# Performance work log

Measured on AMD Instinct MI355X. Metric: run time of the kernel, lower is better.

Reference implementation:

```python
import jax, jax.numpy as jnp
import numpy as np

B, T, F, H = 1024, 512, 64, 128


def setup_inputs() -> dict:
    key = jax.random.key(0)
    ks = jax.random.split(key, 9)
    s_ih = 1.0 / np.sqrt(H)
    inp = {
        "x": jax.random.normal(ks[0], (B, T, F), dtype=jnp.float32),
        # PyTorch GRU packed weights: [3H, F] and [3H, H], gate order (r, z, n)
        "W_ih": jax.random.uniform(ks[1], (3 * H, F), minval=-s_ih, maxval=s_ih, dtype=jnp.float32),
        "W_hh": jax.random.uniform(ks[2], (3 * H, H), minval=-s_ih, maxval=s_ih, dtype=jnp.float32),
        "b_ih": jax.random.uniform(ks[3], (3 * H,), minval=-s_ih, maxval=s_ih, dtype=jnp.float32),
        "b_hh": jax.random.uniform(ks[4], (3 * H,), minval=-s_ih, maxval=s_ih, dtype=jnp.float32),
        "W1": jax.random.uniform(ks[5], (32, H), minval=-1 / np.sqrt(H), maxval=1 / np.sqrt(H), dtype=jnp.float32),
        "b1": jax.random.uniform(ks[6], (32,), minval=-1 / np.sqrt(H), maxval=1 / np.sqrt(H), dtype=jnp.float32),
        "W2": jax.random.uniform(ks[7], (1, 32), minval=-1 / np.sqrt(32), maxval=1 / np.sqrt(32), dtype=jnp.float32),
        "b2": jax.random.uniform(ks[8], (1,), minval=-1 / np.sqrt(32), maxval=1 / np.sqrt(32), dtype=jnp.float32),
    }
    return inp


def _gru_last_hidden(x, W_ih, W_hh, b_ih, b_hh):
    # Precompute input-side gate pre-activations for all timesteps: [B, T, 3H]
    xg = jnp.einsum("btf,gf->btg", x, W_ih) + b_ih
    h0 = jnp.zeros((x.shape[0], W_hh.shape[1]), dtype=x.dtype)

    def step(h, xg_t):
        hg = h @ W_hh.T + b_hh  # [B, 3H]
        xr, xz, xn = jnp.split(xg_t, 3, axis=-1)
        hr, hz, hn = jnp.split(hg, 3, axis=-1)
        r = jax.nn.sigmoid(xr + hr)
        z = jax.nn.sigmoid(xz + hz)
        n = jnp.tanh(xn + r * hn)
        h_new = (1.0 - z) * n + z * h
        return h_new, None

    hT, _ = jax.lax.scan(step, h0, jnp.swapaxes(xg, 0, 1))  # scan over T
    return hT  # [B, H]


def reference(x, W_ih, W_hh, b_ih, b_hh, W1, b1, W2, b2):
    hT = _gru_last_hidden(x, W_ih, W_hh, b_ih, b_hh)
    hidden = jax.nn.relu(hT @ W1.T + b1)  # [B, 32]; dropout is identity at inference
    out = hidden @ W2.T + b2  # [B, 1]
    return out.squeeze(-1)  # [B]
```

## Files before the change

### kernel.cpp

```cpp
#include <hip/hip_runtime.h>
#include <math.h>


#define Bsz  1024
#define Tlen 512
#define Fdim 64
#define Hdim 128
#define Gdim 384
#define NB   8
#define NTHR 512
#define NBLK (Bsz / NB)

typedef __attribute__((ext_vector_type(8))) _Float16 f16x8;
typedef __attribute__((ext_vector_type(4))) _Float16 f16x4;
typedef __attribute__((ext_vector_type(2))) _Float16 f16x2;
typedef __attribute__((ext_vector_type(4))) float    f32x4;

__device__ __forceinline__ float fast_sigmoid(float v) {
    return __builtin_amdgcn_rcpf(1.f + __expf(-v));
}
__device__ __forceinline__ float fast_tanh(float v) {
    return 1.f - 2.f * __builtin_amdgcn_rcpf(__expf(2.f * v) + 1.f);
}

__global__ void
__attribute__((amdgpu_flat_work_group_size(NTHR, NTHR), amdgpu_waves_per_eu(2, 2)))
gru_mfma(const float* __restrict__ x,
         const float* __restrict__ W_ih, const float* __restrict__ W_hh,
         const float* __restrict__ b_ih, const float* __restrict__ b_hh,
         const float* __restrict__ W1, const float* __restrict__ b1,
         const float* __restrict__ W2, const float* __restrict__ b2,
         float* __restrict__ out)
{
    __shared__ __align__(16) _Float16 WH[24 * 4 * 4 * 128];
    __shared__ __align__(16) _Float16 WI[24 * 2 * 4 * 128];
    __shared__ __align__(16) _Float16 U0[6 * 4 * 16 * 8];
    __shared__ __align__(16) _Float16 U1[6 * 4 * 16 * 8];

    const int tid  = threadIdx.x;
    const int w    = tid >> 6;
    const int l    = tid & 63;
    const int q    = l >> 4;
    const int bcol = l & 15;
    const int b0   = blockIdx.x * NB;

    for (int i = tid; i < Gdim * Hdim; i += NTHR) {
        int gr = i >> 7, k = i & 127;
        int idx = (((gr >> 4) * 4 + (k >> 5)) * 4 + ((k & 31) >> 3)) * 128
                + (gr & 15) * 8 + (k & 7);
        WH[idx] = (_Float16)W_hh[i];
    }
    for (int i = tid; i < Gdim * Fdim; i += NTHR) {
        int gr = i >> 6, k = i & 63;
        int idx = (((gr >> 4) * 2 + (k >> 5)) * 4 + ((k & 31) >> 3)) * 128
                + (gr & 15) * 8 + (k & 7);
        WI[idx] = (_Float16)W_ih[i];
    }
    for (int i = tid; i < 6 * 4 * 16 * 8; i += NTHR) { U0[i] = (_Float16)0.f; U1[i] = (_Float16)0.f; }
    if (tid < NB * Fdim / 2) {
        int e = tid * 2, bx_ = e >> 6, j = e & 63;
        float2 xv = *reinterpret_cast<const float2*>(
            &x[((size_t)(b0 + bx_) * Tlen + 0) * Fdim + j]);
        int kk = 128 + j;
        int idx = (((kk >> 5) * 4 + ((kk & 31) >> 3)) * 16 + bx_) * 8 + (kk & 7);
        U0[idx]     = (_Float16)xv.x;
        U0[idx + 1] = (_Float16)xv.y;
    }

    float br[4], bz[4], bnh[4], bnx[4];
    #pragma unroll
    for (int j = 0; j < 4; ++j) {
        int gr = 16 * w + q * 4 + j;
        br[j]  = b_ih[gr] + b_hh[gr];
        bz[j]  = b_ih[Hdim + gr] + b_hh[Hdim + gr];
        bnh[j] = b_hh[2 * Hdim + gr];
        bnx[j] = b_ih[2 * Hdim + gr];
    }

    float hp0 = 0.f, hp1 = 0.f, hp2 = 0.f, hp3 = 0.f;

    const int kb    = 16 * w + 4 * q;
    const int hbase = (((kb >> 5) * 4 + ((kb & 31) >> 3)) * 16 + bcol) * 8 + (kb & 7);

    const bool xthr = (tid < NB * Fdim / 2);
    const int e_x = tid * 2, bx = xthr ? (e_x >> 6) : 0, jx = e_x & 63;
    const int kx  = 128 + jx;
    const int xidx = (((kx >> 5) * 4 + ((kx & 31) >> 3)) * 16 + bx) * 8 + (kx & 7);
    const float* xsrc = &x[(size_t)(b0 + bx) * Tlen * Fdim + jx];

    __syncthreads();

#define WHF(gt, kt) (*reinterpret_cast<const f16x8*>(&WH[((((gt)*4+(kt))*4+q)*128) + (l&15)*8]))
#define WIF(gt, kt) (*reinterpret_cast<const f16x8*>(&WI[((((gt)*2+(kt))*4+q)*128) + (l&15)*8]))
#define MFMA(a, b, c) __builtin_amdgcn_mfma_f32_16x16x32_f16((a), (b), (c), 0, 0, 0)

    f16x8 whr0 = WHF(w, 0),      whr1 = WHF(w, 1),      whr2 = WHF(w, 2),      whr3 = WHF(w, 3);
    f16x8 whz0 = WHF(8 + w, 0),  whz1 = WHF(8 + w, 1),  whz2 = WHF(8 + w, 2),  whz3 = WHF(8 + w, 3);
    f16x8 whn0 = WHF(16 + w, 0), whn1 = WHF(16 + w, 1), whn2 = WHF(16 + w, 2), whn3 = WHF(16 + w, 3);
    f16x8 wir0 = WIF(w, 0),      wir1 = WIF(w, 1);
    f16x8 wiz0 = WIF(8 + w, 0),  wiz1 = WIF(8 + w, 1);
    f16x8 win0 = WIF(16 + w, 0), win1 = WIF(16 + w, 1);

    float2 xp = {0.f, 0.f};
    if (xthr) xp = *reinterpret_cast<const float2*>(xsrc + (size_t)1 * Fdim);

    auto step = [&](const _Float16* __restrict__ Ur, _Float16* __restrict__ Uw, int t) {
        asm volatile("" : "+a"(whr0), "+a"(whr1), "+a"(whr2), "+a"(whr3),
                          "+a"(whz0), "+a"(whz1));
        asm volatile("" : "+a"(whz2), "+a"(whz3), "+a"(whn0), "+a"(whn1),
                          "+a"(whn2), "+a"(whn3));
        asm volatile("" : "+a"(wir0), "+a"(wir1), "+a"(wiz0), "+a"(wiz1),
                          "+a"(win0), "+a"(win1));

        f16x8 ub0 = *reinterpret_cast<const f16x8*>(&Ur[((0*4+q)*16 + bcol)*8]);
        f16x8 ub1 = *reinterpret_cast<const f16x8*>(&Ur[((1*4+q)*16 + bcol)*8]);
        f16x8 ub2 = *reinterpret_cast<const f16x8*>(&Ur[((2*4+q)*16 + bcol)*8]);
        f16x8 ub3 = *reinterpret_cast<const f16x8*>(&Ur[((3*4+q)*16 + bcol)*8]);
        f16x8 ub4 = *reinterpret_cast<const f16x8*>(&Ur[((4*4+q)*16 + bcol)*8]);
        f16x8 ub5 = *reinterpret_cast<const f16x8*>(&Ur[((5*4+q)*16 + bcol)*8]);

        float2 xw = xp;
        if (xthr && t + 2 < Tlen)
            xp = *reinterpret_cast<const float2*>(xsrc + (size_t)(t + 2) * Fdim);

        f32x4 cr  = {br[0],  br[1],  br[2],  br[3]};
        f32x4 cz  = {bz[0],  bz[1],  bz[2],  bz[3]};
        f32x4 cnh = {bnh[0], bnh[1], bnh[2], bnh[3]};
        f32x4 cnx = {bnx[0], bnx[1], bnx[2], bnx[3]};

        cr  = MFMA(whr0, ub0, cr);
        cz  = MFMA(whz0, ub0, cz);
        cnh = MFMA(whn0, ub0, cnh);
        cr  = MFMA(whr1, ub1, cr);
        cz  = MFMA(whz1, ub1, cz);
        cnh = MFMA(whn1, ub1, cnh);
        cr  = MFMA(whr2, ub2, cr);
        cz  = MFMA(whz2, ub2, cz);
        cnh = MFMA(whn2, ub2, cnh);
        cr  = MFMA(whr3, ub3, cr);
        cz  = MFMA(whz3, ub3, cz);
        cnh = MFMA(whn3, ub3, cnh);
        cr  = MFMA(wir0, ub4, cr);
        cz  = MFMA(wiz0, ub4, cz);
        cnx = MFMA(win0, ub4, cnx);
        cr  = MFMA(wir1, ub5, cr);
        cz  = MFMA(wiz1, ub5, cz);
        cnx = MFMA(win1, ub5, cnx);

        float r0 = fast_sigmoid(cr[0]), z0 = fast_sigmoid(cz[0]);
        float r1 = fast_sigmoid(cr[1]), z1 = fast_sigmoid(cz[1]);
        float r2 = fast_sigmoid(cr[2]), z2 = fast_sigmoid(cz[2]);
        float r3 = fast_sigmoid(cr[3]), z3 = fast_sigmoid(cz[3]);
        float n0 = fast_tanh(cnx[0] + r0 * cnh[0]);
        float n1 = fast_tanh(cnx[1] + r1 * cnh[1]);
        float n2 = fast_tanh(cnx[2] + r2 * cnh[2]);
        float n3 = fast_tanh(cnx[3] + r3 * cnh[3]);
        hp0 = n0 + z0 * (hp0 - n0);
        hp1 = n1 + z1 * (hp1 - n1);
        hp2 = n2 + z2 * (hp2 - n2);
        hp3 = n3 + z3 * (hp3 - n3);

        f16x4 hq = {(_Float16)hp0, (_Float16)hp1, (_Float16)hp2, (_Float16)hp3};
        *reinterpret_cast<f16x4*>(&Uw[hbase]) = hq;

        if (xthr && t + 1 < Tlen) {
            f16x2 xq = {(_Float16)xw.x, (_Float16)xw.y};
            *reinterpret_cast<f16x2*>(&Uw[xidx]) = xq;
        }
        __syncthreads();
    };

    #pragma unroll 1
    for (int t = 0; t < Tlen; t += 2) {
        step(U0, U1, t);
        step(U1, U0, t + 1);
    }

    for (int sidx = tid; sidx < 32 * NB; sidx += NTHR) {
        int m = sidx & 31, b = sidx >> 5;
        float acc = b1[m];
        #pragma unroll 8
        for (int k = 0; k < Hdim; ++k) {
            int ui = (((k >> 5) * 4 + ((k & 31) >> 3)) * 16 + b) * 8 + (k & 7);
            acc += W1[m * Hdim + k] * (float)U0[ui];
        }
        float v = W2[m] * fmaxf(acc, 0.f);
        v += __shfl_xor(v, 1,  32);
        v += __shfl_xor(v, 2,  32);
        v += __shfl_xor(v, 4,  32);
        v += __shfl_xor(v, 8,  32);
        v += __shfl_xor(v, 16, 32);
        if (m == 0) out[b0 + b] = v + b2[0];
    }
}

extern "C" void kernel_launch(void* const* d_in, const int* in_sizes, int n_in,
                              void* d_out, int out_size, void* d_ws, size_t ws_size,
                              hipStream_t stream)
{
    const float* x    = (const float*)d_in[0];
    const float* W_ih = (const float*)d_in[1];
    const float* W_hh = (const float*)d_in[2];
    const float* b_ih = (const float*)d_in[3];
    const float* b_hh = (const float*)d_in[4];
    const float* W1   = (const float*)d_in[5];
    const float* b1   = (const float*)d_in[6];
    const float* W2   = (const float*)d_in[7];
    const float* b2   = (const float*)d_in[8];
    float* out = (float*)d_out;

    dim3 grid(NBLK), block(NTHR);
    hipLaunchKernelGGL(gru_mfma, grid, block, 0, stream,
                       x, W_ih, W_hh, b_ih, b_hh, W1, b1, W2, b2, out);
}
```

Before: 343.2 us.

## Fill all 16 MFMA batch columns and pipeline input projection one step ahead

Raises the per-block batch from 8 to 16 so every MFMA column carries a real sample, which halves the grid to 64 blocks. It also computes the input-side gate pre-activations for step t+1 during step t and carries them in registers, taking those MFMAs off the critical dependency chain. The x staging is shifted one step ahead to match, all threads now load x, and U1 is no longer zeroed. The risk is that only 64 of the MI355X's CUs are used, and the deeper x prefetch adds register pressure.

New measurement: 344.3 us. Within noise of the previous version (+0.3%).

```diff
diff --git a/kernel.cpp b/kernel.cpp
--- a/kernel.cpp
+++ b/kernel.cpp
@@ -7,7 +7,7 @@
 #define Fdim 64
 #define Hdim 128
 #define Gdim 384
-#define NB   8
+#define NB   16
 #define NTHR 512
 #define NBLK (Bsz / NB)
 
@@ -56,8 +56,8 @@
                 + (gr & 15) * 8 + (k & 7);
         WI[idx] = (_Float16)W_ih[i];
     }
-    for (int i = tid; i < 6 * 4 * 16 * 8; i += NTHR) { U0[i] = (_Float16)0.f; U1[i] = (_Float16)0.f; }
-    if (tid < NB * Fdim / 2) {
+    for (int i = tid; i < 2048; i += NTHR) U0[i] = (_Float16)0.f;
+    {
         int e = tid * 2, bx_ = e >> 6, j = e & 63;
         float2 xv = *reinterpret_cast<const float2*>(
             &x[((size_t)(b0 + bx_) * Tlen + 0) * Fdim + j]);
@@ -82,8 +82,7 @@
     const int kb    = 16 * w + 4 * q;
     const int hbase = (((kb >> 5) * 4 + ((kb & 31) >> 3)) * 16 + bcol) * 8 + (kb & 7);
 
-    const bool xthr = (tid < NB * Fdim / 2);
-    const int e_x = tid * 2, bx = xthr ? (e_x >> 6) : 0, jx = e_x & 63;
+    const int e_x = tid * 2, bx = e_x >> 6, jx = e_x & 63;
     const int kx  = 128 + jx;
     const int xidx = (((kx >> 5) * 4 + ((kx & 31) >> 3)) * 16 + bx) * 8 + (kx & 7);
     const float* xsrc = &x[(size_t)(b0 + bx) * Tlen * Fdim + jx];
@@ -101,8 +100,26 @@
     f16x8 wiz0 = WIF(8 + w, 0),  wiz1 = WIF(8 + w, 1);
     f16x8 win0 = WIF(16 + w, 0), win1 = WIF(16 + w, 1);
 
-    float2 xp = {0.f, 0.f};
-    if (xthr) xp = *reinterpret_cast<const float2*>(xsrc + (size_t)1 * Fdim);
+    f32x4 cxr, cxz, cxn;
+    {
+        f16x8 ub4 = *reinterpret_cast<const f16x8*>(&U0[((4*4+q)*16 + bcol)*8]);
+        f16x8 ub5 = *reinterpret_cast<const f16x8*>(&U0[((5*4+q)*16 + bcol)*8]);
+        cxr = f32x4{br[0], br[1], br[2], br[3]};
+        cxz = f32x4{bz[0], bz[1], bz[2], bz[3]};
+        cxn = f32x4{bnx[0], bnx[1], bnx[2], bnx[3]};
+        cxr = MFMA(wir0, ub4, cxr); cxr = MFMA(wir1, ub5, cxr);
+        cxz = MFMA(wiz0, ub4, cxz); cxz = MFMA(wiz1, ub5, cxz);
+        cxn = MFMA(win0, ub4, cxn); cxn = MFMA(win1, ub5, cxn);
+    }
+    __syncthreads();
+
+    {
+        float2 x1 = *reinterpret_cast<const float2*>(xsrc + (size_t)1 * Fdim);
+        f16x2 xq = {(_Float16)x1.x, (_Float16)x1.y};
+        *reinterpret_cast<f16x2*>(&U0[xidx]) = xq;
+    }
+    float2 xp = *reinterpret_cast<const float2*>(xsrc + (size_t)2 * Fdim);
+    __syncthreads();
 
     auto step = [&](const _Float16* __restrict__ Ur, _Float16* __restrict__ Uw, int t) {
         asm volatile("" : "+a"(whr0), "+a"(whr1), "+a"(whr2), "+a"(whr3),
@@ -120,13 +137,13 @@
         f16x8 ub5 = *reinterpret_cast<const f16x8*>(&Ur[((5*4+q)*16 + bcol)*8]);
 
         float2 xw = xp;
-        if (xthr && t + 2 < Tlen)
-            xp = *reinterpret_cast<const float2*>(xsrc + (size_t)(t + 2) * Fdim);
-
-        f32x4 cr  = {br[0],  br[1],  br[2],  br[3]};
-        f32x4 cz  = {bz[0],  bz[1],  bz[2],  bz[3]};
+        if (t + 3 < Tlen)
+            xp = *reinterpret_cast<const float2*>(xsrc + (size_t)(t + 3) * Fdim);
+
+        f32x4 cr  = cxr;
+        f32x4 cz  = cxz;
         f32x4 cnh = {bnh[0], bnh[1], bnh[2], bnh[3]};
-        f32x4 cnx = {bnx[0], bnx[1], bnx[2], bnx[3]};
+        f32x4 cnxu = cxn;
 
         cr  = MFMA(whr0, ub0, cr);
         cz  = MFMA(whz0, ub0, cz);
@@ -140,21 +157,22 @@
         cr  = MFMA(whr3, ub3, cr);
         cz  = MFMA(whz3, ub3, cz);
         cnh = MFMA(whn3, ub3, cnh);
-        cr  = MFMA(wir0, ub4, cr);
-        cz  = MFMA(wiz0, ub4, cz);
-        cnx = MFMA(win0, ub4, cnx);
-        cr  = MFMA(wir1, ub5, cr);
-        cz  = MFMA(wiz1, ub5, cz);
-        cnx = MFMA(win1, ub5, cnx);
+
+        cxr = f32x4{br[0], br[1], br[2], br[3]};
+        cxz = f32x4{bz[0], bz[1], bz[2], bz[3]};
+        cxn = f32x4{bnx[0], bnx[1], bnx[2], bnx[3]};
+        cxr = MFMA(wir0, ub4, cxr); cxr = MFMA(wir1, ub5, cxr);
+        cxz = MFMA(wiz0, ub4, cxz); cxz = MFMA(wiz1, ub5, cxz);
+        cxn = MFMA(win0, ub4, cxn); cxn = MFMA(win1, ub5, cxn);
 
         float r0 = fast_sigmoid(cr[0]), z0 = fast_sigmoid(cz[0]);
         float r1 = fast_sigmoid(cr[1]), z1 = fast_sigmoid(cz[1]);
         float r2 = fast_sigmoid(cr[2]), z2 = fast_sigmoid(cz[2]);
         float r3 = fast_sigmoid(cr[3]), z3 = fast_sigmoid(cz[3]);
-        float n0 = fast_tanh(cnx[0] + r0 * cnh[0]);
-        float n1 = fast_tanh(cnx[1] + r1 * cnh[1]);
-        float n2 = fast_tanh(cnx[2] + r2 * cnh[2]);
-        float n3 = fast_tanh(cnx[3] + r3 * cnh[3]);
+        float n0 = fast_tanh(cnxu[0] + r0 * cnh[0]);
+        float n1 = fast_tanh(cnxu[1] + r1 * cnh[1]);
+        float n2 = fast_tanh(cnxu[2] + r2 * cnh[2]);
+        float n3 = fast_tanh(cnxu[3] + r3 * cnh[3]);
         hp0 = n0 + z0 * (hp0 - n0);
         hp1 = n1 + z1 * (hp1 - n1);
         hp2 = n2 + z2 * (hp2 - n2);
@@ -163,7 +181,7 @@
         f16x4 hq = {(_Float16)hp0, (_Float16)hp1, (_Float16)hp2, (_Float16)hp3};
         *reinterpret_cast<f16x4*>(&Uw[hbase]) = hq;
 
-        if (xthr && t + 1 < Tlen) {
+        if (t + 2 < Tlen) {
             f16x2 xq = {(_Float16)xw.x, (_Float16)xw.y};
             *reinterpret_cast<f16x2*>(&Uw[xidx]) = xq;
         }
@@ -176,8 +194,8 @@
         step(U1, U0, t + 1);
     }
 
-    for (int sidx = tid; sidx < 32 * NB; sidx += NTHR) {
-        int m = sidx & 31, b = sidx >> 5;
+    {
+        int m = tid & 31, b = tid >> 5;
         float acc = b1[m];
         #pragma unroll 8
         for (int k = 0; k < Hdim; ++k) {
```
